# Kernel optimization log

Measured on AMD Instinct MI355X. Metric: run time of the kernel, lower is better.

## Reference

```python
import jax, jax.numpy as jnp
import numpy as np

N_SAMPLE, N_ATOMS, N_TOKENS, N_CHAINS = 4, 8192, 1024, 8
AF3_THR = 1.1  # af3_clash_threshold
COUNT_THR = 100  # total_clash > 100
REL_THR = 0.5    # relative_clash > 0.5


def setup_inputs() -> dict:
    key = jax.random.key(0)
    k1, = jax.random.split(key, 1)
    # coords spread out a bit so clashes are sparse-ish but nonzero
    pred_coordinate = jax.random.normal(k1, (N_SAMPLE, N_ATOMS, 3), dtype=jnp.float32) * 5.0
    # balanced sorted chain assignment per token: guarantees all ids 0..N_CHAINS-1 present
    asym_id = ((jnp.arange(N_TOKENS) * N_CHAINS) // N_TOKENS).astype(jnp.int32)
    # monotone atoms -> tokens map (N_ATOMS // N_TOKENS atoms per token)
    atom_to_token_idx = (jnp.arange(N_ATOMS) // (N_ATOMS // N_TOKENS)).astype(jnp.int32)
    return {
        "pred_coordinate": pred_coordinate,
        "asym_id": asym_id,
        "atom_to_token_idx": atom_to_token_idx,
    }


def reference(pred_coordinate, asym_id, atom_to_token_idx):
    # Per-atom chain id, then one-hot chain membership M: [N_atoms, N_chains]
    atom_chain = asym_id[atom_to_token_idx]
    M = jax.nn.one_hot(atom_chain, N_CHAINS, dtype=pred_coordinate.dtype)
    n_per_chain = M.sum(axis=0)  # [C] atoms per chain

    # Squared pairwise distances via gram expansion (avoids [S,N,N,3] diff tensor)
    sq = jnp.sum(pred_coordinate * pred_coordinate, axis=-1)          # [S, N]
    gram = jnp.einsum('snd,smd->snm', pred_coordinate, pred_coordinate)  # [S, N, N]
    d2 = sq[:, :, None] + sq[:, None, :] - 2.0 * gram                 # [S, N, N]

    # dist < thr  <=>  d2 < thr^2 (both non-negative)
    clash = (d2 < AF3_THR * AF3_THR).astype(pred_coordinate.dtype)

    # counts[s, a, b] = #{(i in chain a, j in chain b) : clash}; two small GEMMs
    counts = jnp.einsum('snm,na,mb->sab', clash, M, M)  # [S, C, C]

    # original only fills strict off-diagonal pairs (i < j, mirrored); diagonal stays 0
    off = 1.0 - jnp.eye(N_CHAINS, dtype=counts.dtype)
    total = counts * off
    min_n = jnp.minimum(n_per_chain[:, None], n_per_chain[None, :])
    rel = total / min_n

    af3_clash_details = jnp.stack([total, rel], axis=-1)  # [S, C, C, 2]
    has_af3_clash = (total > COUNT_THR) | (rel > REL_THR)  # [S, C, C] bool
    return has_af3_clash, af3_clash_details
```

## Files before the change

### kernel.cpp

```cpp
#include <hip/hip_runtime.h>

#define NS 4
#define NA 8192
#define NTOK 1024
#define NC 8
#define THREADS 256
#define JSLOTS 4
#define JPB (THREADS * JSLOTS)
#define TI 64
#define TPJ (JPB / TI)
#define GRIDX 448


__global__ __launch_bounds__(THREADS)
void setup_kernel(const float* __restrict__ coords, const int* __restrict__ asym,
                  const int* __restrict__ a2t, float4* __restrict__ staged,
                  int* __restrict__ chain, int* __restrict__ counts) {
  const float THR2 = 1.21f;
  int idx = blockIdx.x * THREADS + threadIdx.x;
  float x = coords[3 * idx + 0], y = coords[3 * idx + 1], z = coords[3 * idx + 2];
  staged[idx] = make_float4(2.0f * x, 2.0f * y, 2.0f * z,
                            2.0f * (THR2 - (x * x + y * y + z * z)));
  if (idx < NA) chain[idx] = asym[a2t[idx]];
  if (idx < NS * NC * NC) counts[idx] = 0;
}

__global__ __launch_bounds__(THREADS, 8)
void clash_kernel(const float4* __restrict__ staged, const int* __restrict__ chain,
                  int* __restrict__ counts) {
  __shared__ int red[NC * NC];

  const int tid = threadIdx.x;
  const int s = blockIdx.z;

  int f = blockIdx.x, jb = 1;
  while (f >= 8 * jb * (jb + 1)) ++jb;
  const int ib = f - 8 * jb * (jb - 1);

  if (tid < NC * NC) red[tid] = 0;

  const float4* __restrict__ sb = staged + (size_t)s * NA;
  const float TWO_THR2 = 2.42f;

  float xj[JSLOTS], yj[JSLOTS], zj[JSLOTS], tj2[JSLOTS];
  int bj[JSLOTS];
#pragma unroll
  for (int u = 0; u < JSLOTS; ++u) {
    int j = jb * JPB + u * THREADS + tid;
    float4 cj = sb[j];
    xj[u] = cj.x; yj[u] = cj.y; zj[u] = cj.z;
    tj2[u] = TWO_THR2 - cj.w;
    bj[u] = chain[j];
  }

  int myi = chain[ib * TI + (tid & 63)];
  const int A = __builtin_amdgcn_readfirstlane(myi);
  bool uniform = __all(myi == A);

  int b0[JSLOTS];
#pragma unroll
  for (int u = 0; u < JSLOTS; ++u) {
    b0[u] = __builtin_amdgcn_readfirstlane(bj[u]);
    uniform = uniform && __all(bj[u] == b0[u]);
  }

  __syncthreads();

  const float4* __restrict__ tg = sb + ib * TI;

  if (uniform) {
    int acc[JSLOTS] = {0, 0, 0, 0};
#pragma unroll 8
    for (int t = 0; t < TI; ++t) {
      float4 ci = tg[t];
#pragma unroll
      for (int u = 0; u < JSLOTS; ++u) {
        float d = fmaf(ci.x, xj[u], fmaf(ci.y, yj[u], fmaf(ci.z, zj[u], ci.w)));
        acc[u] += __popcll(__ballot(d > tj2[u]));
      }
    }
    if ((tid & 63) == 0) {
#pragma unroll
      for (int u = 0; u < JSLOTS; ++u) {
        if (acc[u]) {
          atomicAdd(&red[A * NC + b0[u]], acc[u]);
          atomicAdd(&red[b0[u] * NC + A], acc[u]);
        }
      }
    }
  } else {
    for (int t = 0; t < TI; ++t) {
      float4 ci = tg[t];
      int a = chain[ib * TI + t];
#pragma unroll
      for (int u = 0; u < JSLOTS; ++u) {
        float d = fmaf(ci.x, xj[u], fmaf(ci.y, yj[u], fmaf(ci.z, zj[u], ci.w)));
        if (d > tj2[u]) {
          atomicAdd(&red[a * NC + bj[u]], 1);
          atomicAdd(&red[bj[u] * NC + a], 1);
        }
      }
    }
  }

  __syncthreads();
  if (tid < NC * NC) {
    int v = red[tid];
    if (v) atomicAdd(&counts[s * NC * NC + tid], v);
  }
}

__global__ __launch_bounds__(THREADS)
void finalize_kernel(const int* __restrict__ asym, const int* __restrict__ counts,
                     float* __restrict__ out) {
  __shared__ int hist[NC];
  int tid = threadIdx.x;
  if (tid < NC) hist[tid] = 0;
  __syncthreads();
  for (int t = tid; t < NTOK; t += THREADS) atomicAdd(&hist[asym[t]], NA / NTOK);
  __syncthreads();

  int c = counts[tid];
  int a = (tid >> 3) & 7, b = tid & 7;
  float total = (a == b) ? 0.0f : (float)c;
  float minn = (float)min(hist[a], hist[b]);
  float rel = total / minn;
  out[tid] = ((total > 100.0f) || (rel > 0.5f)) ? 1.0f : 0.0f;
  out[256 + 2 * tid + 0] = total;
  out[256 + 2 * tid + 1] = rel;
}

extern "C" void kernel_launch(void* const* d_in, const int* in_sizes, int n_in,
                              void* d_out, int out_size, void* d_ws, size_t ws_size,
                              hipStream_t stream) {
  const float* coords = (const float*)d_in[0];
  const int* asym = (const int*)d_in[1];
  const int* a2t = (const int*)d_in[2];
  float* out = (float*)d_out;

  float4* staged = (float4*)d_ws;
  int* chain = (int*)(staged + NS * NA);
  int* counts = chain + NA;

  setup_kernel<<<dim3(NS * NA / THREADS), THREADS, 0, stream>>>(coords, asym, a2t,
                                                                staged, chain, counts);
  clash_kernel<<<dim3(GRIDX, 1, NS), THREADS, 0, stream>>>(staged, chain, counts);
  finalize_kernel<<<1, THREADS, 0, stream>>>(asym, counts, out);
}
```

Measured before the change: 77.53 us.

## Fuse finalize into clash kernel via last-block pattern and use packed FMA

```diff
diff --git a/kernel.cpp b/kernel.cpp
--- a/kernel.cpp
+++ b/kernel.cpp
@@ -10,6 +10,9 @@
 #define TI 64
 #define TPJ (JPB / TI)
 #define GRIDX 448
+#define NBLOCKS (GRIDX * NS)
+
+typedef float v2f __attribute__((ext_vector_type(2)));
 
 
 __global__ __launch_bounds__(THREADS)
@@ -22,16 +25,20 @@
   staged[idx] = make_float4(2.0f * x, 2.0f * y, 2.0f * z,
                             2.0f * (THR2 - (x * x + y * y + z * z)));
   if (idx < NA) chain[idx] = asym[a2t[idx]];
-  if (idx < NS * NC * NC) counts[idx] = 0;
+  if (idx < NS * NC * NC + 1) counts[idx] = 0;
 }
 
-__global__ __launch_bounds__(THREADS, 8)
+__global__ __launch_bounds__(THREADS, 7)
 void clash_kernel(const float4* __restrict__ staged, const int* __restrict__ chain,
-                  int* __restrict__ counts) {
+                  const int* __restrict__ asym, int* __restrict__ counts,
+                  float* __restrict__ out) {
   __shared__ int red[NC * NC];
+  __shared__ int hist[NC];
+  __shared__ int lastFlag;
 
   const int tid = threadIdx.x;
   const int s = blockIdx.z;
+  int* done = counts + NS * NC * NC;
 
   int f = blockIdx.x, jb = 1;
   while (f >= 8 * jb * (jb + 1)) ++jb;
@@ -42,14 +49,16 @@
   const float4* __restrict__ sb = staged + (size_t)s * NA;
   const float TWO_THR2 = 2.42f;
 
-  float xj[JSLOTS], yj[JSLOTS], zj[JSLOTS], tj2[JSLOTS];
+  v2f jx2[2], jy2[2], jz2[2], jt2[2];
   int bj[JSLOTS];
 #pragma unroll
   for (int u = 0; u < JSLOTS; ++u) {
     int j = jb * JPB + u * THREADS + tid;
     float4 cj = sb[j];
-    xj[u] = cj.x; yj[u] = cj.y; zj[u] = cj.z;
-    tj2[u] = TWO_THR2 - cj.w;
+    jx2[u >> 1][u & 1] = cj.x;
+    jy2[u >> 1][u & 1] = cj.y;
+    jz2[u >> 1][u & 1] = cj.z;
+    jt2[u >> 1][u & 1] = TWO_THR2 - cj.w;
     bj[u] = chain[j];
   }
 
@@ -73,10 +82,15 @@
 #pragma unroll 8
     for (int t = 0; t < TI; ++t) {
       float4 ci = tg[t];
+      v2f cx = {ci.x, ci.x}, cy = {ci.y, ci.y};
+      v2f cz = {ci.z, ci.z}, cw = {ci.w, ci.w};
 #pragma unroll
-      for (int u = 0; u < JSLOTS; ++u) {
-        float d = fmaf(ci.x, xj[u], fmaf(ci.y, yj[u], fmaf(ci.z, zj[u], ci.w)));
-        acc[u] += __popcll(__ballot(d > tj2[u]));
+      for (int p = 0; p < 2; ++p) {
+        v2f d = __builtin_elementwise_fma(cx, jx2[p],
+                __builtin_elementwise_fma(cy, jy2[p],
+                __builtin_elementwise_fma(cz, jz2[p], cw)));
+        acc[2 * p + 0] += __popcll(__ballot(d.x > jt2[p].x));
+        acc[2 * p + 1] += __popcll(__ballot(d.y > jt2[p].y));
       }
     }
     if ((tid & 63) == 0) {
@@ -94,8 +108,10 @@
       int a = chain[ib * TI + t];
 #pragma unroll
       for (int u = 0; u < JSLOTS; ++u) {
-        float d = fmaf(ci.x, xj[u], fmaf(ci.y, yj[u], fmaf(ci.z, zj[u], ci.w)));
-        if (d > tj2[u]) {
+        float xu = jx2[u >> 1][u & 1], yu = jy2[u >> 1][u & 1];
+        float zu = jz2[u >> 1][u & 1], tu = jt2[u >> 1][u & 1];
+        float d = fmaf(ci.x, xu, fmaf(ci.y, yu, fmaf(ci.z, zu, ci.w)));
+        if (d > tu) {
           atomicAdd(&red[a * NC + bj[u]], 1);
           atomicAdd(&red[bj[u] * NC + a], 1);
         }
@@ -108,19 +124,20 @@
     int v = red[tid];
     if (v) atomicAdd(&counts[s * NC * NC + tid], v);
   }
-}
 
-__global__ __launch_bounds__(THREADS)
-void finalize_kernel(const int* __restrict__ asym, const int* __restrict__ counts,
-                     float* __restrict__ out) {
-  __shared__ int hist[NC];
-  int tid = threadIdx.x;
+  __threadfence();
+  __syncthreads();
+  if (tid == 0) lastFlag = (atomicAdd(done, 1) == NBLOCKS - 1);
+  __syncthreads();
+  if (!lastFlag) return;
+
   if (tid < NC) hist[tid] = 0;
   __syncthreads();
   for (int t = tid; t < NTOK; t += THREADS) atomicAdd(&hist[asym[t]], NA / NTOK);
   __syncthreads();
 
-  int c = counts[tid];
+  __threadfence();
+  int c = atomicAdd(&counts[tid], 0);
   int a = (tid >> 3) & 7, b = tid & 7;
   float total = (a == b) ? 0.0f : (float)c;
   float minn = (float)min(hist[a], hist[b]);
@@ -144,6 +161,6 @@
 
   setup_kernel<<<dim3(NS * NA / THREADS), THREADS, 0, stream>>>(coords, asym, a2t,
                                                                 staged, chain, counts);
-  clash_kernel<<<dim3(GRIDX, 1, NS), THREADS, 0, stream>>>(staged, chain, counts);
-  finalize_kernel<<<1, THREADS, 0, stream>>>(asym, counts, out);
+  clash_kernel<<<dim3(GRIDX, 1, NS), THREADS, 0, stream>>>(staged, chain, asym,
+                                                           counts, out);
 }
```

New measurement: 169.6 us. 2.19x slower.
